# Performance work log

Hardware: AMD Instinct MI355X
Metric: run time of the kernel (lower is better)

## Reference

```python
import jax, jax.numpy as jnp
import numpy as np

NQ = 4          # n_qubits
NL = 3          # n_reservoir_layers (data re-uploading layers)
K = 25          # decomposition kernel size
SEQ = 168
PRED = 96
C_FEAT = 64
B = 4096
LAG_IDX = (167, 166, 165, 164, 163, 162, 145, 144, 143, 1, 0)  # seq_len - lag


def _apply_ry_batched(state, theta, q):
    # state: (B, 2,2,2,2) complex; theta: (B,) per-sample RY angle on qubit q
    c = jnp.cos(theta * 0.5)
    s = jnp.sin(theta * 0.5)
    m = jnp.moveaxis(state, q + 1, -1)
    shp = (-1,) + (1,) * (m.ndim - 2)
    c = c.reshape(shp)
    s = s.reshape(shp)
    a0, a1 = m[..., 0], m[..., 1]
    m = jnp.stack([c * a0 - s * a1, s * a0 + c * a1], axis=-1)
    return jnp.moveaxis(m, -1, q + 1)


def _rot_matrix(phi, theta, omega):
    # PennyLane Rot = RZ(omega) @ RY(theta) @ RZ(phi)
    ct = jnp.cos(theta * 0.5)
    st = jnp.sin(theta * 0.5)
    ep = jnp.exp(-0.5j * (phi + omega))
    em = jnp.exp(0.5j * (phi - omega))
    return jnp.stack([jnp.stack([ep * ct, -em * st]),
                      jnp.stack([jnp.conj(em) * st, jnp.conj(ep) * ct])])


def _apply_1q(state, U, q):
    m = jnp.moveaxis(state, q + 1, -1)
    m = jnp.einsum('...i,ji->...j', m, U)
    return jnp.moveaxis(m, -1, q + 1)


def _cnot(state, c, t):
    m = jnp.moveaxis(state, (c + 1, t + 1), (1, 2))
    m = jnp.stack([m[:, 0], jnp.flip(m[:, 1], axis=1)], axis=1)
    return jnp.moveaxis(m, (1, 2), (c + 1, t + 1))


def _run_circuit(inputs, weights):
    # inputs: (B, NQ) angles; weights: (NL, NQ, 3) Rot params; per-layer: data
    # re-upload AngleEmbedding(RY) + 1-layer StronglyEntanglingLayers (range=1)
    b = inputs.shape[0]
    state = jnp.zeros((b,) + (2,) * NQ, jnp.complex64)
    state = state.at[(slice(None),) + (0,) * NQ].set(1.0)
    for l in range(NL):
        for q in range(NQ):
            state = _apply_ry_batched(state, inputs[:, q], q)
        for q in range(NQ):
            U = _rot_matrix(weights[l, q, 0], weights[l, q, 1], weights[l, q, 2])
            state = _apply_1q(state, U, q)
        for q in range(NQ):
            state = _cnot(state, q, (q + 1) % NQ)
    return state


def _expvals(state, pauli):
    outs = []
    for q in range(NQ):
        m = jnp.moveaxis(state, q + 1, 1)
        a0 = m[:, 0].reshape(m.shape[0], -1)
        a1 = m[:, 1].reshape(m.shape[0], -1)
        if pauli == 'X':
            outs.append(2.0 * jnp.real(jnp.sum(jnp.conj(a0) * a1, axis=1)))
        elif pauli == 'Y':
            outs.append(2.0 * jnp.imag(jnp.sum(jnp.conj(a0) * a1, axis=1)))
        else:  # Z
            outs.append(jnp.sum(jnp.abs(a0) ** 2 - jnp.abs(a1) ** 2, axis=1))
    return jnp.stack(outs, axis=-1)  # (B, NQ)


def _decomp(x, w):
    # Adaptive (learnable, softmax-normalized) per-channel moving average with
    # replicate padding (DLinear-style); seasonal = x - trend.
    b, L, c = x.shape
    pad = (K - 1) // 2
    xc = jnp.transpose(x, (0, 2, 1))                       # (B,C,L)
    xp = jnp.pad(xc, ((0, 0), (0, 0), (pad, pad)), mode='edge')
    ker = jax.nn.softmax(w, axis=-1)[:, None, :]           # (C,1,K)
    trend = jax.lax.conv_general_dilated(
        xp, ker, (1,), 'VALID',
        dimension_numbers=('NCH', 'OIH', 'NCH'), feature_group_count=c)
    trend = jnp.transpose(trend, (0, 2, 1))                # (B,L,C)
    return x - trend, trend


def setup_inputs() -> dict:
    key = jax.random.key(0)
    ks = jax.random.split(key, 16)
    n_lags = len(LAG_IDX)
    two_pi = 2.0 * np.pi
    inp = {
        'x': jax.random.normal(ks[0], (B, SEQ, C_FEAT), jnp.float32),
        'decomp_w': jax.random.normal(ks[1], (C_FEAT, K), jnp.float32) * 0.02,
        'trend_W': jax.random.normal(ks[2], (PRED, SEQ), jnp.float32) * (1.0 / np.sqrt(SEQ)),
        'trend_b': jnp.zeros((PRED,), jnp.float32),
        'seas_W': jax.random.normal(ks[3], (PRED, SEQ), jnp.float32) * (1.0 / np.sqrt(SEQ)),
        'seas_b': jnp.zeros((PRED,), jnp.float32),
        'lagc_W': jax.random.normal(ks[4], (NQ, n_lags), jnp.float32) * (1.0 / np.sqrt(n_lags)),
        'lagc_b': jnp.zeros((NQ,), jnp.float32),
        'res_wx': jax.random.uniform(ks[5], (NL, NQ, 3), jnp.float32, 0.0, two_pi),
        'res_wy': jax.random.uniform(ks[6], (NL, NQ, 3), jnp.float32, 0.0, two_pi),
        'res_wz': jax.random.uniform(ks[7], (NL, NQ, 3), jnp.float32, 0.0, two_pi),
        'ro_W1': jax.random.normal(ks[8], (3 * NQ, 3 * NQ), jnp.float32) * (1.0 / np.sqrt(3 * NQ)),
        'ro_b1': jnp.zeros((3 * NQ,), jnp.float32),
        'ro_W2': jax.random.normal(ks[9], (PRED, 3 * NQ), jnp.float32) * (1.0 / np.sqrt(3 * NQ)),
        'ro_b2': jnp.zeros((PRED,), jnp.float32),
        'alpha': jnp.array([0.5], jnp.float32),
    }
    return inp


def reference(x, decomp_w, trend_W, trend_b, seas_W, seas_b, lagc_W, lagc_b,
              res_wx, res_wy, res_wz, ro_W1, ro_b1, ro_W2, ro_b2, alpha):
    seasonal, trend = _decomp(x, decomp_w)
    trend_out = jnp.einsum('blc,pl->bpc', trend, trend_W) + trend_b[None, :, None]
    seas_base = jnp.einsum('blc,pl->bpc', seasonal, seas_W) + seas_b[None, :, None]
    lag = x[:, jnp.array(LAG_IDX), -1]                      # (B, n_lags)
    q_in = jnp.tanh(lag @ lagc_W.T + lagc_b) * jnp.float32(np.pi)
    feats = jnp.concatenate([
        _expvals(_run_circuit(q_in, res_wx), 'X'),
        _expvals(_run_circuit(q_in, res_wy), 'Y'),
        _expvals(_run_circuit(q_in, res_wz), 'Z')], axis=-1)  # (B, 12)
    h = jax.nn.relu(feats @ ro_W1.T + ro_b1)
    mod = jnp.tanh(h @ ro_W2.T + ro_b2)                     # (B, PRED); dropout off (eval)
    seas_out = seas_base * (1.0 + mod[:, :, None])
    a = jax.nn.sigmoid(alpha[0])
    return a * seas_out + (1.0 - a) * trend_out
```

## Files before the change

kernel.cpp:

```cpp
#include <hip/hip_runtime.h>
#include <math.h>

#define BB   4096
#define SEQL 168
#define CF   64
#define PREDN 96
#define KK   25
#define NLAG 11
#define LSTR 178

#define WS_KER   0
#define WS_U     1600
#define WS_FEATS 2048
#define WS_SWZ   51200

typedef __attribute__((ext_vector_type(8))) short short8;
typedef __attribute__((ext_vector_type(4))) float f32x4;

__device__ __forceinline__ unsigned short f2bf(float f) {
    unsigned int u = __float_as_uint(f);
    u = (u + 0x7FFFu + ((u >> 16) & 1u)) >> 16;
    return (unsigned short)u;
}

__global__ void k_pre(const float* __restrict__ decomp_w,
                      const float* __restrict__ wx,
                      const float* __restrict__ wy,
                      const float* __restrict__ wz,
                      float* __restrict__ ws)
{
    int tid = threadIdx.x;
    if (tid < 64) {
        float v[KK]; float mx = -1e30f;
        #pragma unroll
        for (int k = 0; k < KK; ++k) { v[k] = decomp_w[tid*KK + k]; mx = fmaxf(mx, v[k]); }
        float s = 0.f;
        #pragma unroll
        for (int k = 0; k < KK; ++k) { v[k] = expf(v[k] - mx); s += v[k]; }
        float inv = 1.f / s;
        #pragma unroll
        for (int k = 0; k < KK; ++k) ws[WS_KER + tid*KK + k] = v[k]*inv;
    } else if (tid < 64 + 36) {
        int i = tid - 64;
        int circ = i / 12, r = i % 12;
        const float* w = (circ == 0) ? wx : (circ == 1 ? wy : wz);
        float phi = w[r*3+0], th = w[r*3+1], om = w[r*3+2];
        float ct = cosf(0.5f*th), st = sinf(0.5f*th);
        float po = 0.5f*(phi+om), pm = 0.5f*(phi-om);
        float cpo = cosf(po), spo = sinf(po);
        float cpm = cosf(pm), spm = sinf(pm);
        float* U = ws + WS_U + i*8;
        U[0] =  cpo*ct; U[1] = -spo*ct;
        U[2] = -cpm*st; U[3] = -spm*st;
        U[4] =  cpm*st; U[5] = -spm*st;
        U[6] =  cpo*ct; U[7] =  spo*ct;
    }
}

__global__ void k_swz(const float* __restrict__ sW,
                      const float* __restrict__ tW,
                      const float* __restrict__ alpha,
                      float* __restrict__ ws)
{
    int idx = blockIdx.x * blockDim.x + threadIdx.x;
    if (idx >= 2*6*6*64*8) return;
    float oma = 1.f - 1.f/(1.f + expf(-alpha[0]));
    unsigned short* wsw = (unsigned short*)(ws + WS_SWZ);
    int j    = idx & 7;
    int lane = (idx >> 3) & 63;
    int rem  = idx >> 9;
    int ks   = rem % 6;
    int nt   = (rem / 6) % 6;
    int mat  = rem / 36;
    int p = nt*16 + (lane & 15);
    int l = ks*32 + ((lane >> 4) & 3)*8 + j;
    float v = 0.f;
    if (l < SEQL) v = mat ? oma * tW[p*SEQL + l] : sW[p*SEQL + l];
    wsw[idx] = f2bf(v);
}

__global__ void k_quantum(const float* __restrict__ x,
                          const float* __restrict__ lagc_W,
                          const float* __restrict__ lagc_b,
                          const float* __restrict__ ws,
                          float* __restrict__ feats)
{
    int tid  = blockIdx.x * blockDim.x + threadIdx.x;
    int unit = tid >> 4;
    int amp  = tid & 15;
    int b = unit / 3, circ = unit - b*3;

    const int LAGS[NLAG] = {167,166,165,164,163,162,145,144,143,1,0};
    const float* xb = x + (size_t)b*SEQL*CF + (CF-1);
    float lag[NLAG];
    #pragma unroll
    for (int j = 0; j < NLAG; ++j) lag[j] = xb[LAGS[j]*CF];

    float cq[4], sq[4];
    #pragma unroll
    for (int q = 0; q < 4; ++q) {
        float acc = lagc_b[q];
        #pragma unroll
        for (int j = 0; j < NLAG; ++j) acc = fmaf(lag[j], lagc_W[q*NLAG + j], acc);
        float half = 0.5f * 3.14159265358979323846f * tanhf(acc);
        cq[q] = cosf(half); sq[q] = sinf(half);
    }

    float sr = (amp == 0) ? 1.f : 0.f;
    float si = 0.f;

    const float* Ub = ws + WS_U + circ*96;

    for (int layer = 0; layer < 3; ++layer) {
        #pragma unroll
        for (int q = 0; q < 4; ++q) {
            int m = 1 << (3-q);
            float pr  = __shfl_xor(sr, m);
            float pii = __shfl_xor(si, m);
            float sel = (amp & m) ? sq[q] : -sq[q];
            sr = fmaf(sel, pr,  cq[q]*sr);
            si = fmaf(sel, pii, cq[q]*si);
        }
        #pragma unroll
        for (int q = 0; q < 4; ++q) {
            const float* U = Ub + (layer*4 + q)*8;
            int m = 1 << (3-q);
            bool hi = (amp & m) != 0;
            float uar = hi ? U[6] : U[0];
            float uai = hi ? U[7] : U[1];
            float ubr = hi ? U[4] : U[2];
            float ubi = hi ? U[5] : U[3];
            float pr  = __shfl_xor(sr, m);
            float pii = __shfl_xor(si, m);
            float nr = uar*sr - uai*si + ubr*pr - ubi*pii;
            float ni = uar*si + uai*sr + ubr*pii + ubi*pr;
            sr = nr; si = ni;
        }
        #pragma unroll
        for (int q = 0; q < 4; ++q) {
            int t  = (q+1) & 3;
            int cm = 1 << (3-q), tm = 1 << (3-t);
            float pr  = __shfl_xor(sr, tm);
            float pii = __shfl_xor(si, tm);
            if (amp & cm) { sr = pr; si = pii; }
        }
    }

    #pragma unroll
    for (int q = 0; q < 4; ++q) {
        int m = 1 << (3-q);
        float pr  = __shfl_xor(sr, m);
        float pii = __shfl_xor(si, m);
        float v;
        if (circ == 0) {
            v = sr*pr + si*pii;
        } else if (circ == 1) {
            float t = sr*pii - si*pr;
            v = (amp & m) ? -t : t;
        } else {
            float t = sr*sr + si*si;
            v = (amp & m) ? -t : t;
        }
        v += __shfl_xor(v, 1);
        v += __shfl_xor(v, 2);
        v += __shfl_xor(v, 4);
        v += __shfl_xor(v, 8);
        if (amp == 0) feats[b*12 + circ*4 + q] = v;
    }
}

__launch_bounds__(256, 3)
__global__ void k_gemm(const float* __restrict__ x,
                       const float* __restrict__ ws,
                       const float* __restrict__ seas_b,
                       const float* __restrict__ trend_b,
                       const float* __restrict__ roW1,
                       const float* __restrict__ rob1,
                       const float* __restrict__ roW2,
                       const float* __restrict__ rob2,
                       const float* __restrict__ alpha,
                       float* __restrict__ out)
{
    __shared__ unsigned short lbuf[2*64*LSTR + 64];
    __shared__ float fsL[PREDN];
    __shared__ float cbL[PREDN];

    int b = blockIdx.x;
    int tid = threadIdx.x;

    float a_sig = 1.f / (1.f + expf(-alpha[0]));
    float oma   = 1.f - a_sig;

    if (tid < PREDN) {
        const float* f = ws + WS_FEATS + b*12;
        float h[12];
        #pragma unroll
        for (int i = 0; i < 12; ++i) {
            float acc = rob1[i];
            #pragma unroll
            for (int j = 0; j < 12; ++j) acc = fmaf(roW1[i*12+j], f[j], acc);
            h[i] = fmaxf(acc, 0.f);
        }
        float acc = rob2[tid];
        #pragma unroll
        for (int i = 0; i < 12; ++i) acc = fmaf(roW2[tid*12+i], h[i], acc);
        float m   = tanhf(acc);
        float fsv = a_sig * (1.f + m);
        fsL[tid] = fsv;
        cbL[tid] = fsv*seas_b[tid] + oma*trend_b[tid];
    }

    for (int i = tid; i < 2*64*10 + 64; i += 256) {
        if (i < 2*64*10) {
            int arr = i / 640;
            int rem = i - arr*640;
            int c   = rem / 10;
            int l   = 168 + rem - c*10;
            lbuf[arr*64*LSTR + c*LSTR + l] = 0;
        } else {
            lbuf[2*64*LSTR + (i - 2*64*10)] = 0;
        }
    }

    {
        int c   = tid & 63;
        int seg = tid >> 6;
        float cf[KK];
        #pragma unroll
        for (int k = 0; k < KK; ++k) cf[k] = ws[WS_KER + c*KK + k];
        const float* xc = x + (size_t)b*SEQL*CF + c;
        unsigned short* lT = lbuf + c*LSTR;
        unsigned short* lS = lbuf + 64*LSTR + c*LSTR;

        int l0 = seg*42;
        float w[KK];
        #pragma unroll
        for (int k = 0; k < KK; ++k) {
            int ix = l0 + k - 12;
            ix = ix < 0 ? 0 : (ix > SEQL-1 ? SEQL-1 : ix);
            w[k] = xc[ix*CF];
        }
        #pragma unroll
        for (int l = 0; l < 42; ++l) {
            int ll = l0 + l;
            float acc = 0.f;
            #pragma unroll
            for (int k = 0; k < KK; ++k) acc = fmaf(cf[k], w[k], acc);
            lT[ll] = f2bf(acc);
            lS[ll] = f2bf(w[12] - acc);
            #pragma unroll
            for (int k = 0; k < KK-1; ++k) w[k] = w[k+1];
            int ix = ll + 13;
            ix = ix > SEQL-1 ? SEQL-1 : ix;
            w[KK-1] = xc[ix*CF];
        }
    }
    __syncthreads();

    int lane = tid & 63;
    int ct   = tid >> 6;
    int mrow = lane & 15;
    int q    = lane >> 4;
    int c    = ct*16 + mrow;

    const unsigned int* L32 = (const unsigned int*)lbuf;
    const int SOFF = 64*LSTR/2;
    const unsigned short* wsw = (const unsigned short*)(ws + WS_SWZ);

    f32x4 accS[6], accT[6];
    #pragma unroll
    for (int nt = 0; nt < 6; ++nt) {
        accS[nt] = (f32x4){0.f,0.f,0.f,0.f};
        accT[nt] = (f32x4){0.f,0.f,0.f,0.f};
    }

    for (int ks = 0; ks < 6; ++ks) {
        int ai = c*(LSTR/2) + ks*16 + q*4;
        union { unsigned int u[4]; short8 v; } ut, us;
        #pragma unroll
        for (int d = 0; d < 4; ++d) {
            ut.u[d] = L32[ai + d];
            us.u[d] = L32[SOFF + ai + d];
        }
        short8 aT = ut.v, aS = us.v;
        #pragma unroll
        for (int nt = 0; nt < 6; ++nt) {
            short8 Bs = *(const short8*)(wsw + (((0*6 + nt)*6 + ks)*64 + lane)*8);
            short8 Bt = *(const short8*)(wsw + (((1*6 + nt)*6 + ks)*64 + lane)*8);
            accS[nt] = __builtin_amdgcn_mfma_f32_16x16x32_bf16(aS, Bs, accS[nt], 0, 0, 0);
            accT[nt] = __builtin_amdgcn_mfma_f32_16x16x32_bf16(aT, Bt, accT[nt], 0, 0, 0);
        }
    }

    #pragma unroll
    for (int nt = 0; nt < 6; ++nt) {
        int p = nt*16 + mrow;
        float fsv = fsL[p];
        float cbv = cbL[p];
        float* og = out + (size_t)b*PREDN*CF + p*CF + ct*16 + (q<<2);
        f32x4 r;
        #pragma unroll
        for (int r4 = 0; r4 < 4; ++r4)
            r[r4] = fmaf(fsv, accS[nt][r4], accT[nt][r4] + cbv);
        *(f32x4*)og = r;
    }
}

extern "C" void kernel_launch(void* const* d_in, const int* in_sizes, int n_in,
                              void* d_out, int out_size, void* d_ws, size_t ws_size,
                              hipStream_t stream)
{
    const float* x        = (const float*)d_in[0];
    const float* decomp_w = (const float*)d_in[1];
    const float* trend_W  = (const float*)d_in[2];
    const float* trend_b  = (const float*)d_in[3];
    const float* seas_W   = (const float*)d_in[4];
    const float* seas_b   = (const float*)d_in[5];
    const float* lagc_W   = (const float*)d_in[6];
    const float* lagc_b   = (const float*)d_in[7];
    const float* res_wx   = (const float*)d_in[8];
    const float* res_wy   = (const float*)d_in[9];
    const float* res_wz   = (const float*)d_in[10];
    const float* ro_W1    = (const float*)d_in[11];
    const float* ro_b1    = (const float*)d_in[12];
    const float* ro_W2    = (const float*)d_in[13];
    const float* ro_b2    = (const float*)d_in[14];
    const float* alpha    = (const float*)d_in[15];
    float* out = (float*)d_out;
    float* ws  = (float*)d_ws;

    k_pre<<<1, 128, 0, stream>>>(decomp_w, res_wx, res_wy, res_wz, ws);
    k_swz<<<144, 256, 0, stream>>>(seas_W, trend_W, alpha, ws);
    k_quantum<<<768, 256, 0, stream>>>(x, lagc_W, lagc_b, ws, ws + WS_FEATS);
    k_gemm<<<BB, 256, 0, stream>>>(x, ws, seas_b, trend_b,
                                   ro_W1, ro_b1, ro_W2, ro_b2, alpha, out);
}
```

Measured before the change: 357.9 us.

## Split GEMM warps by matrix and N-tile, exchange trend results via LDS

Each wave now computes one matrix (seasonal or trend) for three N-tiles across all four channel tiles, instead of both matrices for six N-tiles over one channel tile. This reduces the global loads of swizzled B weights per wave, since each B fragment is reused across four MFMAs, at the cost of more LDS A-fragment reads. Trend accumulators are written to shared memory and read back by the seasonal waves for the fused epilogue. This adds two barriers, and only half the waves perform the output stores.

After: 343.3 us. 4.1% less time.

```diff
diff --git a/kernel.cpp b/kernel.cpp
--- a/kernel.cpp
+++ b/kernel.cpp
@@ -181,7 +181,7 @@
                        const float* __restrict__ alpha,
                        float* __restrict__ out)
 {
-    __shared__ unsigned short lbuf[2*64*LSTR + 64];
+    __shared__ __align__(16) unsigned short lbuf[2*64*LSTR + 64];
     __shared__ float fsL[PREDN];
     __shared__ float cbL[PREDN];
 
@@ -258,51 +258,74 @@
     __syncthreads();
 
     int lane = tid & 63;
-    int ct   = tid >> 6;
+    int wid  = tid >> 6;
     int mrow = lane & 15;
     int q    = lane >> 4;
-    int c    = ct*16 + mrow;
+    int matT = wid >> 1;
+    int ntb  = (wid & 1)*3;
 
     const unsigned int* L32 = (const unsigned int*)lbuf;
     const int SOFF = 64*LSTR/2;
+    const int AOFF = matT ? 0 : SOFF;
     const unsigned short* wsw = (const unsigned short*)(ws + WS_SWZ);
 
-    f32x4 accS[6], accT[6];
+    f32x4 acc[3][4];
     #pragma unroll
-    for (int nt = 0; nt < 6; ++nt) {
-        accS[nt] = (f32x4){0.f,0.f,0.f,0.f};
-        accT[nt] = (f32x4){0.f,0.f,0.f,0.f};
-    }
+    for (int n3 = 0; n3 < 3; ++n3)
+        #pragma unroll
+        for (int ct = 0; ct < 4; ++ct)
+            acc[n3][ct] = (f32x4){0.f,0.f,0.f,0.f};
 
     for (int ks = 0; ks < 6; ++ks) {
-        int ai = c*(LSTR/2) + ks*16 + q*4;
-        union { unsigned int u[4]; short8 v; } ut, us;
-        #pragma unroll
-        for (int d = 0; d < 4; ++d) {
-            ut.u[d] = L32[ai + d];
-            us.u[d] = L32[SOFF + ai + d];
-        }
-        short8 aT = ut.v, aS = us.v;
-        #pragma unroll
-        for (int nt = 0; nt < 6; ++nt) {
-            short8 Bs = *(const short8*)(wsw + (((0*6 + nt)*6 + ks)*64 + lane)*8);
-            short8 Bt = *(const short8*)(wsw + (((1*6 + nt)*6 + ks)*64 + lane)*8);
-            accS[nt] = __builtin_amdgcn_mfma_f32_16x16x32_bf16(aS, Bs, accS[nt], 0, 0, 0);
-            accT[nt] = __builtin_amdgcn_mfma_f32_16x16x32_bf16(aT, Bt, accT[nt], 0, 0, 0);
-        }
-    }
-
-    #pragma unroll
-    for (int nt = 0; nt < 6; ++nt) {
-        int p = nt*16 + mrow;
-        float fsv = fsL[p];
-        float cbv = cbL[p];
-        float* og = out + (size_t)b*PREDN*CF + p*CF + ct*16 + (q<<2);
-        f32x4 r;
-        #pragma unroll
-        for (int r4 = 0; r4 < 4; ++r4)
-            r[r4] = fmaf(fsv, accS[nt][r4], accT[nt][r4] + cbv);
-        *(f32x4*)og = r;
+        short8 a[4];
+        #pragma unroll
+        for (int ct = 0; ct < 4; ++ct) {
+            int ai = AOFF + (ct*16 + mrow)*(LSTR/2) + ks*16 + q*4;
+            union { unsigned int u[4]; short8 v; } ua;
+            #pragma unroll
+            for (int d = 0; d < 4; ++d) ua.u[d] = L32[ai + d];
+            a[ct] = ua.v;
+        }
+        #pragma unroll
+        for (int n3 = 0; n3 < 3; ++n3) {
+            short8 Bv = *(const short8*)(wsw + (((matT*6 + ntb + n3)*6 + ks)*64 + lane)*8);
+            #pragma unroll
+            for (int ct = 0; ct < 4; ++ct)
+                acc[n3][ct] = __builtin_amdgcn_mfma_f32_16x16x32_bf16(a[ct], Bv, acc[n3][ct], 0, 0, 0);
+        }
+    }
+
+    __syncthreads();
+    float* tbuf = (float*)lbuf;
+    if (matT) {
+        int half = wid & 1;
+        #pragma unroll
+        for (int n3 = 0; n3 < 3; ++n3)
+            #pragma unroll
+            for (int ct = 0; ct < 4; ++ct)
+                #pragma unroll
+                for (int r = 0; r < 4; ++r)
+                    tbuf[((n3*4+ct)*4+r)*128 + half*64 + lane] = acc[n3][ct][r];
+    }
+    __syncthreads();
+    if (!matT) {
+        #pragma unroll
+        for (int n3 = 0; n3 < 3; ++n3) {
+            int p = (ntb + n3)*16 + mrow;
+            float fsv = fsL[p];
+            float cbv = cbL[p];
+            #pragma unroll
+            for (int ct = 0; ct < 4; ++ct) {
+                float* og = out + (size_t)b*PREDN*CF + p*CF + ct*16 + (q<<2);
+                f32x4 r;
+                #pragma unroll
+                for (int r4 = 0; r4 < 4; ++r4) {
+                    float tv = tbuf[((n3*4+ct)*4+r4)*128 + wid*64 + lane];
+                    r[r4] = fmaf(fsv, acc[n3][ct][r4], tv + cbv);
+                }
+                *(f32x4*)og = r;
+            }
+        }
     }
 }
 
```

## Split k_gemm across 512 threads with one wave per S/T matrix

Applied to the files above, without the earlier changes.

Doubles the k_gemm block to 512 threads. The decomposition convolution is split into eight 21-step segments instead of four 42-step ones. In the MFMA stage each wave now computes only the seasonal or only the trend product, so per-wave accumulators and A-fragment loads are halved. The trend results are handed to the seasonal waves through LDS (reusing lbuf) before the fused epilogue. The aim is more waves in flight and lower register pressure per wave, at the cost of two extra barriers and an LDS round-trip for the accumulators.

Measured after the change: 653.0 us. 82.5% more time.

```diff
diff --git a/kernel.cpp b/kernel.cpp
--- a/kernel.cpp
+++ b/kernel.cpp
@@ -169,7 +169,7 @@
     }
 }
 
-__launch_bounds__(256, 3)
+__launch_bounds__(512, 6)
 __global__ void k_gemm(const float* __restrict__ x,
                        const float* __restrict__ ws,
                        const float* __restrict__ seas_b,
@@ -181,7 +181,7 @@
                        const float* __restrict__ alpha,
                        float* __restrict__ out)
 {
-    __shared__ unsigned short lbuf[2*64*LSTR + 64];
+    __shared__ __align__(16) unsigned short lbuf[2*64*LSTR + 64];
     __shared__ float fsL[PREDN];
     __shared__ float cbL[PREDN];
 
@@ -210,7 +210,7 @@
         cbL[tid] = fsv*seas_b[tid] + oma*trend_b[tid];
     }
 
-    for (int i = tid; i < 2*64*10 + 64; i += 256) {
+    for (int i = tid; i < 2*64*10 + 64; i += 512) {
         if (i < 2*64*10) {
             int arr = i / 640;
             int rem = i - arr*640;
@@ -232,7 +232,7 @@
         unsigned short* lT = lbuf + c*LSTR;
         unsigned short* lS = lbuf + 64*LSTR + c*LSTR;
 
-        int l0 = seg*42;
+        int l0 = seg*21;
         float w[KK];
         #pragma unroll
         for (int k = 0; k < KK; ++k) {
@@ -241,7 +241,7 @@
             w[k] = xc[ix*CF];
         }
         #pragma unroll
-        for (int l = 0; l < 42; ++l) {
+        for (int l = 0; l < 21; ++l) {
             int ll = l0 + l;
             float acc = 0.f;
             #pragma unroll
@@ -258,51 +258,60 @@
     __syncthreads();
 
     int lane = tid & 63;
-    int ct   = tid >> 6;
+    int wave = tid >> 6;
+    int ct   = wave >> 1;
+    int mat  = wave & 1;
     int mrow = lane & 15;
     int q    = lane >> 4;
     int c    = ct*16 + mrow;
 
     const unsigned int* L32 = (const unsigned int*)lbuf;
     const int SOFF = 64*LSTR/2;
+    const int AOFF = mat ? 0 : SOFF;
     const unsigned short* wsw = (const unsigned short*)(ws + WS_SWZ);
 
-    f32x4 accS[6], accT[6];
+    f32x4 acc[6];
     #pragma unroll
-    for (int nt = 0; nt < 6; ++nt) {
-        accS[nt] = (f32x4){0.f,0.f,0.f,0.f};
-        accT[nt] = (f32x4){0.f,0.f,0.f,0.f};
-    }
+    for (int nt = 0; nt < 6; ++nt) acc[nt] = (f32x4){0.f,0.f,0.f,0.f};
 
     for (int ks = 0; ks < 6; ++ks) {
-        int ai = c*(LSTR/2) + ks*16 + q*4;
-        union { unsigned int u[4]; short8 v; } ut, us;
-        #pragma unroll
-        for (int d = 0; d < 4; ++d) {
-            ut.u[d] = L32[ai + d];
-            us.u[d] = L32[SOFF + ai + d];
-        }
-        short8 aT = ut.v, aS = us.v;
+        int ai = AOFF + c*(LSTR/2) + ks*16 + q*4;
+        union { unsigned int u[4]; short8 v; } ua;
+        #pragma unroll
+        for (int d = 0; d < 4; ++d) ua.u[d] = L32[ai + d];
+        short8 a = ua.v;
         #pragma unroll
         for (int nt = 0; nt < 6; ++nt) {
-            short8 Bs = *(const short8*)(wsw + (((0*6 + nt)*6 + ks)*64 + lane)*8);
-            short8 Bt = *(const short8*)(wsw + (((1*6 + nt)*6 + ks)*64 + lane)*8);
-            accS[nt] = __builtin_amdgcn_mfma_f32_16x16x32_bf16(aS, Bs, accS[nt], 0, 0, 0);
-            accT[nt] = __builtin_amdgcn_mfma_f32_16x16x32_bf16(aT, Bt, accT[nt], 0, 0, 0);
-        }
-    }
-
-    #pragma unroll
-    for (int nt = 0; nt < 6; ++nt) {
-        int p = nt*16 + mrow;
-        float fsv = fsL[p];
-        float cbv = cbL[p];
-        float* og = out + (size_t)b*PREDN*CF + p*CF + ct*16 + (q<<2);
-        f32x4 r;
-        #pragma unroll
-        for (int r4 = 0; r4 < 4; ++r4)
-            r[r4] = fmaf(fsv, accS[nt][r4], accT[nt][r4] + cbv);
-        *(f32x4*)og = r;
+            short8 Bv = *(const short8*)(wsw + (((mat*6 + nt)*6 + ks)*64 + lane)*8);
+            acc[nt] = __builtin_amdgcn_mfma_f32_16x16x32_bf16(a, Bv, acc[nt], 0, 0, 0);
+        }
+    }
+
+    __syncthreads();
+    float* tbuf = (float*)lbuf;
+    if (mat) {
+        #pragma unroll
+        for (int nt = 0; nt < 6; ++nt)
+            #pragma unroll
+            for (int r = 0; r < 4; ++r)
+                tbuf[((ct*6+nt)*4+r)*64 + lane] = acc[nt][r];
+    }
+    __syncthreads();
+    if (!mat) {
+        #pragma unroll
+        for (int nt = 0; nt < 6; ++nt) {
+            int p = nt*16 + mrow;
+            float fsv = fsL[p];
+            float cbv = cbL[p];
+            float* og = out + (size_t)b*PREDN*CF + p*CF + ct*16 + (q<<2);
+            f32x4 r;
+            #pragma unroll
+            for (int r4 = 0; r4 < 4; ++r4) {
+                float tv = tbuf[((ct*6+nt)*4+r4)*64 + lane];
+                r[r4] = fmaf(fsv, acc[nt][r4], tv + cbv);
+            }
+            *(f32x4*)og = r;
+        }
     }
 }
 
@@ -332,6 +341,6 @@
     k_pre<<<1, 128, 0, stream>>>(decomp_w, res_wx, res_wy, res_wz, ws);
     k_swz<<<144, 256, 0, stream>>>(seas_W, trend_W, alpha, ws);
     k_quantum<<<768, 256, 0, stream>>>(x, lagc_W, lagc_b, ws, ws + WS_FEATS);
-    k_gemm<<<BB, 256, 0, stream>>>(x, ws, seas_b, trend_b,
+    k_gemm<<<BB, 512, 0, stream>>>(x, ws, seas_b, trend_b,
                                    ro_W1, ro_b1, ro_W2, ro_b2, alpha, out);
 }
```

## Compute decomposition directly into MFMA A-fragments in registers, dropping LDS staging

Applied to the files above, without the earlier changes.

Each lane now computes the trend and seasonal moving-average values for its own channel and a contiguous 48-step slice of the sequence. It packs them as bf16 directly into the A operands of the MFMA, so the shared-memory buffer and its zero-padding are gone. The reduction dimension is remapped so that lane group q covers positions q*48 onward, and the weight swizzle is permuted to match. This removes LDS traffic and per-thread bank conflicts but makes each lane compute 48 outputs and hold 48 packed registers. Launch bounds are raised to 4 blocks per SM, which risks register spills.

Result: slower. 628.3 us (+75.5%).

```diff
diff --git a/kernel.cpp b/kernel.cpp
--- a/kernel.cpp
+++ b/kernel.cpp
@@ -7,7 +7,6 @@
 #define PREDN 96
 #define KK   25
 #define NLAG 11
-#define LSTR 178
 
 #define WS_KER   0
 #define WS_U     1600
@@ -73,7 +72,7 @@
     int nt   = (rem / 6) % 6;
     int mat  = rem / 36;
     int p = nt*16 + (lane & 15);
-    int l = ks*32 + ((lane >> 4) & 3)*8 + j;
+    int l = ((lane >> 4) & 3)*48 + ks*8 + j;
     float v = 0.f;
     if (l < SEQL) v = mat ? oma * tW[p*SEQL + l] : sW[p*SEQL + l];
     wsw[idx] = f2bf(v);
@@ -169,7 +168,7 @@
     }
 }
 
-__launch_bounds__(256, 3)
+__launch_bounds__(256, 4)
 __global__ void k_gemm(const float* __restrict__ x,
                        const float* __restrict__ ws,
                        const float* __restrict__ seas_b,
@@ -181,12 +180,16 @@
                        const float* __restrict__ alpha,
                        float* __restrict__ out)
 {
-    __shared__ unsigned short lbuf[2*64*LSTR + 64];
     __shared__ float fsL[PREDN];
     __shared__ float cbL[PREDN];
 
     int b = blockIdx.x;
     int tid = threadIdx.x;
+    int lane = tid & 63;
+    int ct   = tid >> 6;
+    int mrow = lane & 15;
+    int q    = lane >> 4;
+    int c    = ct*16 + mrow;
 
     float a_sig = 1.f / (1.f + expf(-alpha[0]));
     float oma   = 1.f - a_sig;
@@ -209,62 +212,61 @@
         fsL[tid] = fsv;
         cbL[tid] = fsv*seas_b[tid] + oma*trend_b[tid];
     }
-
-    for (int i = tid; i < 2*64*10 + 64; i += 256) {
-        if (i < 2*64*10) {
-            int arr = i / 640;
-            int rem = i - arr*640;
-            int c   = rem / 10;
-            int l   = 168 + rem - c*10;
-            lbuf[arr*64*LSTR + c*LSTR + l] = 0;
-        } else {
-            lbuf[2*64*LSTR + (i - 2*64*10)] = 0;
-        }
-    }
-
-    {
-        int c   = tid & 63;
-        int seg = tid >> 6;
-        float cf[KK];
-        #pragma unroll
-        for (int k = 0; k < KK; ++k) cf[k] = ws[WS_KER + c*KK + k];
-        const float* xc = x + (size_t)b*SEQL*CF + c;
-        unsigned short* lT = lbuf + c*LSTR;
-        unsigned short* lS = lbuf + 64*LSTR + c*LSTR;
-
-        int l0 = seg*42;
-        float w[KK];
-        #pragma unroll
-        for (int k = 0; k < KK; ++k) {
-            int ix = l0 + k - 12;
-            ix = ix < 0 ? 0 : (ix > SEQL-1 ? SEQL-1 : ix);
-            w[k] = xc[ix*CF];
-        }
-        #pragma unroll
-        for (int l = 0; l < 42; ++l) {
-            int ll = l0 + l;
-            float acc = 0.f;
+    __syncthreads();
+
+    float cf[KK];
+    #pragma unroll
+    for (int k = 0; k < KK; ++k) cf[k] = ws[WS_KER + c*KK + k];
+    const float* xc = x + (size_t)b*SEQL*CF + c;
+    int l0 = q*48;
+
+    float w[KK];
+    #pragma unroll
+    for (int k = 0; k < KK; ++k) {
+        int ix = l0 + k - 12;
+        ix = ix < 0 ? 0 : (ix > SEQL-1 ? SEQL-1 : ix);
+        w[k] = xc[ix*CF];
+    }
+
+    unsigned int fT[6][4], fS[6][4];
+    #pragma unroll
+    for (int ks = 0; ks < 6; ++ks) {
+        #pragma unroll
+        for (int d = 0; d < 4; ++d) {
+            unsigned int tlo, thi, slo, shi;
+            {
+                float acc = 0.f;
+                #pragma unroll
+                for (int k = 0; k < KK; ++k) acc = fmaf(cf[k], w[k], acc);
+                tlo = f2bf(acc);
+                slo = f2bf(w[12] - acc);
+                #pragma unroll
+                for (int k = 0; k < KK-1; ++k) w[k] = w[k+1];
+                int ix = l0 + ks*8 + 2*d + 13;
+                ix = ix > SEQL-1 ? SEQL-1 : ix;
+                w[KK-1] = xc[ix*CF];
+            }
+            {
+                float acc = 0.f;
+                #pragma unroll
+                for (int k = 0; k < KK; ++k) acc = fmaf(cf[k], w[k], acc);
+                thi = f2bf(acc);
+                shi = f2bf(w[12] - acc);
+                #pragma unroll
+                for (int k = 0; k < KK-1; ++k) w[k] = w[k+1];
+                int ix = l0 + ks*8 + 2*d + 14;
+                ix = ix > SEQL-1 ? SEQL-1 : ix;
+                w[KK-1] = xc[ix*CF];
+            }
+            fT[ks][d] = tlo | (thi << 16);
+            fS[ks][d] = slo | (shi << 16);
+        }
+        if (l0 + ks*8 >= SEQL) {
             #pragma unroll
-            for (int k = 0; k < KK; ++k) acc = fmaf(cf[k], w[k], acc);
-            lT[ll] = f2bf(acc);
-            lS[ll] = f2bf(w[12] - acc);
-            #pragma unroll
-            for (int k = 0; k < KK-1; ++k) w[k] = w[k+1];
-            int ix = ll + 13;
-            ix = ix > SEQL-1 ? SEQL-1 : ix;
-            w[KK-1] = xc[ix*CF];
-        }
-    }
-    __syncthreads();
-
-    int lane = tid & 63;
-    int ct   = tid >> 6;
-    int mrow = lane & 15;
-    int q    = lane >> 4;
-    int c    = ct*16 + mrow;
-
-    const unsigned int* L32 = (const unsigned int*)lbuf;
-    const int SOFF = 64*LSTR/2;
+            for (int d = 0; d < 4; ++d) { fT[ks][d] = 0; fS[ks][d] = 0; }
+        }
+    }
+
     const unsigned short* wsw = (const unsigned short*)(ws + WS_SWZ);
 
     f32x4 accS[6], accT[6];
@@ -274,14 +276,11 @@
         accT[nt] = (f32x4){0.f,0.f,0.f,0.f};
     }
 
+    #pragma unroll
     for (int ks = 0; ks < 6; ++ks) {
-        int ai = c*(LSTR/2) + ks*16 + q*4;
         union { unsigned int u[4]; short8 v; } ut, us;
         #pragma unroll
-        for (int d = 0; d < 4; ++d) {
-            ut.u[d] = L32[ai + d];
-            us.u[d] = L32[SOFF + ai + d];
-        }
+        for (int d = 0; d < 4; ++d) { ut.u[d] = fT[ks][d]; us.u[d] = fS[ks][d]; }
         short8 aT = ut.v, aS = us.v;
         #pragma unroll
         for (int nt = 0; nt < 6; ++nt) {
```
